# Optimization experiments

Hardware: AMD Instinct MI355X
Metric: run time of the kernel (lower is better)

Reference implementation:

```python
import jax, jax.numpy as jnp
import numpy as np

N = 100000      # num nodes
E = 1600000     # num edges (avg degree 16)
D_IN = 128
D_OUT = 128
EPS = 1e-12     # F.normalize default eps


def setup_inputs() -> dict:
    key = jax.random.key(0)
    k1, k2, k3, k4 = jax.random.split(key, 4)
    x = jax.random.normal(k1, (N, D_IN), dtype=jnp.float32)
    row = jax.random.randint(k2, (E,), 0, N, dtype=jnp.int32)
    # guarantee no self loops in the raw graph: col = (row + offset) % N, offset in [1, N)
    offset = jax.random.randint(k3, (E,), 1, N, dtype=jnp.int32)
    col = (row + offset) % N
    edge_index = jnp.stack([row, col], axis=0)
    # xavier_uniform_ for weight [in, out]
    a = np.sqrt(6.0 / (D_IN + D_OUT)).astype(np.float32)
    weight = jax.random.uniform(k4, (D_IN, D_OUT), dtype=jnp.float32, minval=-a, maxval=a)
    return {"x": x, "edge_index": edge_index, "weight": weight}


def reference(x, edge_index, weight):
    row, col = edge_index[0], edge_index[1]
    # remove_self_loops: drop edges with row == col (mask keeps shapes static)
    mask = (row != col)
    # linear transform first (as in the original forward)
    xw = jnp.matmul(x, weight)                               # [N, D_OUT]
    # scatter_mean over edges with self loops added:
    # out[i] = (sum_{j->i, j!=i} xw[j] + xw[i]) / (deg_nonself(i) + 1)
    msg = jnp.where(mask[:, None], xw[col], jnp.float32(0.0))  # [E, D_OUT]
    seg_sum = jax.ops.segment_sum(msg, row, num_segments=N) + xw
    cnt = jax.ops.segment_sum(mask.astype(xw.dtype), row, num_segments=N) + jnp.float32(1.0)
    out = seg_sum / cnt[:, None]
    # F.normalize(out, p=2, dim=-1): out / max(||out||_2, eps)
    norm = jnp.sqrt(jnp.sum(out * out, axis=-1, keepdims=True))
    out = out / jnp.maximum(norm, jnp.float32(EPS))
    return out
```

## Files before the change

### kernel.cpp

```cpp
#include <hip/hip_runtime.h>
#include <hip/hip_fp16.h>
#include <stdint.h>

#define NN 100000
#define NE 1600000
#define DD 128
#define NTP 100032

#define NBKT 391
#define CAPB 4480
#define GCAP 1024

typedef _Float16 f16x8 __attribute__((ext_vector_type(8)));
typedef float f32x4 __attribute__((ext_vector_type(4)));

__device__ __forceinline__ uint32_t hadd2u(uint32_t a, uint32_t b){
  union { uint32_t u; __half2 h; } x, y;
  x.u = a; y.u = b;
  x.h = __hadd2(x.h, y.h);
  return x.u;
}
__device__ __forceinline__ uint32_t hmul2u(uint32_t a, __half2 m){
  union { uint32_t u; __half2 h; } x; x.u = a;
  x.h = __hmul2(x.h, m);
  return x.u;
}

__global__ __launch_bounds__(256) void k_convert(
    const float4* __restrict__ x, uint2* __restrict__ x16,
    const float* __restrict__ w, uint16_t* __restrict__ wsw){
  int b = blockIdx.x, t = threadIdx.x;
  if (b < 12500){
    int i = b*256 + t;
    float4 v = x[i];
    union { _Float16 h[4]; uint2 u; } r;
    r.h[0] = (_Float16)v.x; r.h[1] = (_Float16)v.y;
    r.h[2] = (_Float16)v.z; r.h[3] = (_Float16)v.w;
    x16[i] = r.u;
  } else {
    int wi = (b - 12500)*256 + t;
    int j = wi & 7, l = (wi >> 3) & 63, kt = (wi >> 9) & 3, ct = wi >> 11;
    int k = kt*32 + ((l >> 4) & 3)*8 + j;
    int d = ct*16 + (l & 15);
    union { _Float16 h; uint16_t u; } cv; cv.h = (_Float16)w[k*DD + d];
    wsw[wi] = cv.u;
  }
}

__global__ __launch_bounds__(256) void k_part1(const int* __restrict__ ei,
                                               int* __restrict__ bktres,
                                               uint32_t* __restrict__ ibuf){
  __shared__ int sh[NBKT];
  int t = threadIdx.x;
  int e0 = blockIdx.x*4096;
  for (int i=t; i<NBKT; i+=256) sh[i] = 0;
  __syncthreads();
  int rr[16], cc[16];
  #pragma unroll
  for (int j=0;j<16;j++){
    int e = e0 + j*256 + t;
    rr[j] = -1;
    if (e < NE){
      rr[j] = ei[e]; cc[j] = ei[NE + e];
      atomicAdd(&sh[rr[j] >> 8], 1);
    }
  }
  __syncthreads();
  for (int i=t; i<NBKT; i+=256){
    int v = sh[i];
    sh[i] = v ? atomicAdd(&bktres[i*16], v) : 0;
  }
  __syncthreads();
  #pragma unroll
  for (int j=0;j<16;j++){
    if (rr[j] >= 0){
      int bk = rr[j] >> 8;
      int p = atomicAdd(&sh[bk], 1);
      if (p < CAPB)
        ibuf[(size_t)bk*CAPB + p] = (uint32_t)(((rr[j] & 255) << 17) | cc[j]);
    }
  }
}

__global__ __launch_bounds__(256) void k_part2(const int* __restrict__ bktres,
                                               uint32_t* __restrict__ ibuf,
                                               uint32_t* __restrict__ rowinfo){
  __shared__ uint32_t s_rec[CAPB];
  __shared__ int s_deg[256], s_off[256], s_cur[256];
  int t = threadIdx.x, lane = t & 63, wid = t >> 6;
  int b = blockIdx.x;
  int cnt = bktres[b*16]; if (cnt > CAPB) cnt = CAPB;
  size_t bb = (size_t)b*CAPB;
  s_deg[t] = 0;
  __syncthreads();
  for (int i=t; i<cnt; i+=256){
    uint32_t rec = ibuf[bb + i];
    s_rec[i] = rec;
    atomicAdd(&s_deg[rec >> 17], 1);
  }
  __syncthreads();
  if (wid == 0){
    int carry = 0;
    for (int ch=0; ch<4; ch++){
      int idx = ch*64 + lane;
      int o = s_deg[idx], v = o;
      #pragma unroll
      for (int d=1; d<64; d<<=1){ int y = __shfl_up(v, d); if (lane >= d) v += y; }
      int ex = carry + v - o;
      s_off[idx] = ex; s_cur[idx] = ex;
      carry += __shfl(v, 63);
    }
  }
  __syncthreads();
  int dgc = s_deg[t] > 255 ? 255 : s_deg[t];
  rowinfo[b*256 + t] = ((uint32_t)s_off[t] << 8) | (uint32_t)dgc;
  for (int i=t; i<cnt; i+=256){
    uint32_t rec = s_rec[i];
    int p = atomicAdd(&s_cur[rec >> 17], 1);
    ibuf[bb + p] = rec & 0x1FFFFu;
  }
}

__global__ __launch_bounds__(256) void k_bin_gather(
    const uint2* __restrict__ xp, const uint32_t* __restrict__ ibuf,
    const uint32_t* __restrict__ rowinfo, uint16_t* __restrict__ agg){
  __shared__ int s_col[GCAP];
  __shared__ int s_loc[32], s_deg[32];
  int t = threadIdx.x, wid = t >> 6, lane = t & 63;
  int b = blockIdx.x;
  int row0 = b << 5;
  if (t < 32){
    uint32_t info = rowinfo[row0 + t];
    s_loc[t] = (int)(info >> 8);
    s_deg[t] = (int)(info & 255u);
  }
  __syncthreads();
  int base = s_loc[0];
  int len = s_loc[31] + s_deg[31] - base; if (len > GCAP) len = GCAP;
  size_t bb = (size_t)(row0 >> 8)*CAPB + base;
  for (int i=t; i<len; i+=256) s_col[i] = (int)ibuf[bb + i];
  __syncthreads();
  int q = lane & 31, half = lane >> 5;
  for (int lr = wid; lr < 32; lr += 4){
    int n = row0 + lr;
    int dg  = s_deg[lr];
    int off = s_loc[lr] - base;
    uint2 sv = xp[(size_t)n*32 + q];
    uint32_t a01 = 0u, a23 = 0u;
    int j = 0;
    for (; j+16 <= dg; j += 16){
      int c0 = s_col[off+j+half],    c1 = s_col[off+j+2+half];
      int c2 = s_col[off+j+4+half],  c3 = s_col[off+j+6+half];
      int c4 = s_col[off+j+8+half],  c5 = s_col[off+j+10+half];
      int c6 = s_col[off+j+12+half], c7 = s_col[off+j+14+half];
      uint2 v0 = xp[(size_t)c0*32 + q]; uint2 v1 = xp[(size_t)c1*32 + q];
      uint2 v2 = xp[(size_t)c2*32 + q]; uint2 v3 = xp[(size_t)c3*32 + q];
      uint2 v4 = xp[(size_t)c4*32 + q]; uint2 v5 = xp[(size_t)c5*32 + q];
      uint2 v6 = xp[(size_t)c6*32 + q]; uint2 v7 = xp[(size_t)c7*32 + q];
      a01 = hadd2u(a01, v0.x); a23 = hadd2u(a23, v0.y);
      a01 = hadd2u(a01, v1.x); a23 = hadd2u(a23, v1.y);
      a01 = hadd2u(a01, v2.x); a23 = hadd2u(a23, v2.y);
      a01 = hadd2u(a01, v3.x); a23 = hadd2u(a23, v3.y);
      a01 = hadd2u(a01, v4.x); a23 = hadd2u(a23, v4.y);
      a01 = hadd2u(a01, v5.x); a23 = hadd2u(a23, v5.y);
      a01 = hadd2u(a01, v6.x); a23 = hadd2u(a23, v6.y);
      a01 = hadd2u(a01, v7.x); a23 = hadd2u(a23, v7.y);
    }
    for (; j+8 <= dg; j += 8){
      int c0 = s_col[off+j+half],   c1 = s_col[off+j+2+half];
      int c2 = s_col[off+j+4+half], c3 = s_col[off+j+6+half];
      uint2 v0 = xp[(size_t)c0*32 + q]; uint2 v1 = xp[(size_t)c1*32 + q];
      uint2 v2 = xp[(size_t)c2*32 + q]; uint2 v3 = xp[(size_t)c3*32 + q];
      a01 = hadd2u(a01, v0.x); a23 = hadd2u(a23, v0.y);
      a01 = hadd2u(a01, v1.x); a23 = hadd2u(a23, v1.y);
      a01 = hadd2u(a01, v2.x); a23 = hadd2u(a23, v2.y);
      a01 = hadd2u(a01, v3.x); a23 = hadd2u(a23, v3.y);
    }
    for (; j+2 <= dg; j += 2){
      int c0 = s_col[off+j+half];
      uint2 v0 = xp[(size_t)c0*32 + q];
      a01 = hadd2u(a01, v0.x); a23 = hadd2u(a23, v0.y);
    }
    if (j < dg){
      int c0 = s_col[off+j];
      uint2 v0 = xp[(size_t)c0*32 + q];
      a01 = hadd2u(a01, half ? 0u : v0.x);
      a23 = hadd2u(a23, half ? 0u : v0.y);
    }
    a01 = hadd2u(a01, (uint32_t)__shfl_xor((int)a01, 32));
    a23 = hadd2u(a23, (uint32_t)__shfl_xor((int)a23, 32));
    __half2 inv2 = __float2half2_rn(1.0f / (float)(dg + 1));
    uint32_t r01 = hmul2u(hadd2u(a01, sv.x), inv2);
    uint32_t r23 = hmul2u(hadd2u(a23, sv.y), inv2);
    uint32_t pair = half ? r23 : r01;
    int k0 = q*4 + half*2;
    int kt = k0 >> 5, gk = (k0 >> 3) & 3, jj = k0 & 7;
    int ld = (n & 15) + (gk << 4);
    *(uint32_t*)(agg + ((((size_t)(n >> 4)*4 + kt)*64 + ld)*8 + jj)) = pair;
  }
}

__global__ __launch_bounds__(256) void k_gemm(const uint16_t* __restrict__ agg,
                                              const uint16_t* __restrict__ wsw,
                                              float* __restrict__ out){
  int tid = threadIdx.x, wid = tid >> 6, lane = tid & 63;
  int g = blockIdx.x*4 + wid;
  const f16x8* A = (const f16x8*)agg;
  const f16x8* B = (const f16x8*)wsw;
  size_t ab = (size_t)g*256 + lane;
  f16x8 a0 = A[ab], a1 = A[ab+64], a2 = A[ab+128], a3 = A[ab+192];

  f32x4 acc[8];
  #pragma unroll
  for (int ct=0;ct<8;ct++) acc[ct] = (f32x4){0.f,0.f,0.f,0.f};
  #pragma unroll
  for (int ct=0;ct<8;ct++){
    acc[ct] = __builtin_amdgcn_mfma_f32_16x16x32_f16(a0, B[(ct*4+0)*64 + lane], acc[ct], 0, 0, 0);
    acc[ct] = __builtin_amdgcn_mfma_f32_16x16x32_f16(a1, B[(ct*4+1)*64 + lane], acc[ct], 0, 0, 0);
    acc[ct] = __builtin_amdgcn_mfma_f32_16x16x32_f16(a2, B[(ct*4+2)*64 + lane], acc[ct], 0, 0, 0);
    acc[ct] = __builtin_amdgcn_mfma_f32_16x16x32_f16(a3, B[(ct*4+3)*64 + lane], acc[ct], 0, 0, 0);
  }

  float sq[4] = {0.f,0.f,0.f,0.f};
  #pragma unroll
  for (int ct=0;ct<8;ct++){
    #pragma unroll
    for (int i=0;i<4;i++) sq[i] += acc[ct][i]*acc[ct][i];
  }
  #pragma unroll
  for (int m=1;m<16;m<<=1){
    #pragma unroll
    for (int i=0;i<4;i++) sq[i] += __shfl_xor(sq[i], m);
  }
  float sc[4];
  #pragma unroll
  for (int i=0;i<4;i++) sc[i] = 1.0f / fmaxf(sqrtf(sq[i]), 1e-12f);

  int col = lane & 15;
  int rb = g*16 + ((lane >> 4) << 2);
  #pragma unroll
  for (int i=0;i<4;i++){
    int n = rb + i;
    if (n < NN){
      #pragma unroll
      for (int ct=0;ct<8;ct++)
        out[(size_t)n*DD + (ct<<4) + col] = acc[ct][i]*sc[i];
    }
  }
}

extern "C" void kernel_launch(void* const* d_in, const int* in_sizes, int n_in,
                              void* d_out, int out_size, void* d_ws, size_t ws_size,
                              hipStream_t stream){
  const float* x = (const float*)d_in[0];
  const int*  ei = (const int*)d_in[1];
  const float* w = (const float*)d_in[2];
  float* out = (float*)d_out;
  char* ws = (char*)d_ws;
  (void)in_sizes; (void)n_in; (void)out_size; (void)ws_size;

  size_t off = 0;
  uint16_t* x16 = (uint16_t*)(ws + off); off += (size_t)NN*DD*2;
  uint16_t* agg = (uint16_t*)(ws + off); off += (size_t)NTP*DD*2;
  uint16_t* wsw = (uint16_t*)(ws + off); off += (size_t)DD*DD*2;
  uint32_t* ibuf = (uint32_t*)(ws + off); off += (size_t)NBKT*CAPB*4;
  int* bktres   = (int*)(ws + off); off += (size_t)NBKT*16*4;
  uint32_t* rowinfo = (uint32_t*)(ws + off); off += (size_t)NBKT*256*4;

  hipMemsetAsync(bktres, 0, (size_t)NBKT*16*4, stream);
  k_convert<<<12564, 256, 0, stream>>>((const float4*)x, (uint2*)x16, w, wsw);
  k_part1<<<391, 256, 0, stream>>>(ei, bktres, ibuf);
  k_part2<<<391, 256, 0, stream>>>(bktres, ibuf, rowinfo);
  k_bin_gather<<<3125, 256, 0, stream>>>((const uint2*)x16, ibuf, rowinfo, agg);
  k_gemm<<<1563, 256, 0, stream>>>(agg, wsw, out);
}
```

Measured before the change: 144.1 us.

## Fuse gather with GEMM through shared memory and merge partition with convert

Merges the fp16 convert kernel with the edge-bucketing pass into one launch. The neighbour-mean gather now also performs the MFMA GEMM and L2 normalisation, keeping the aggregated tile in LDS instead of writing it to global memory and reading it back. Each pair of waves splits the output columns, and partial row norms are combined through shared memory. The gather inner loop is also widened to 32 edges per step, with more loads in flight. This removes two launches and a global round-trip, at the cost of extra LDS, an added barrier, and more register pressure in the gather.

```diff
diff --git a/kernel.cpp b/kernel.cpp
--- a/kernel.cpp
+++ b/kernel.cpp
@@ -5,10 +5,10 @@
 #define NN 100000
 #define NE 1600000
 #define DD 128
-#define NTP 100032
 
 #define NBKT 391
 #define CAPB 4480
+#define NBIN 3125
 #define GCAP 1024
 
 typedef _Float16 f16x8 __attribute__((ext_vector_type(8)));
@@ -26,59 +26,55 @@
   return x.u;
 }
 
-__global__ __launch_bounds__(256) void k_convert(
+__global__ __launch_bounds__(256) void k_front(
+    const int* __restrict__ ei, int* __restrict__ bktres, uint32_t* __restrict__ ibuf,
     const float4* __restrict__ x, uint2* __restrict__ x16,
     const float* __restrict__ w, uint16_t* __restrict__ wsw){
   int b = blockIdx.x, t = threadIdx.x;
-  if (b < 12500){
-    int i = b*256 + t;
+  if (b < NBKT){
+    __shared__ int sh[NBKT];
+    int e0 = b*4096;
+    for (int i=t; i<NBKT; i+=256) sh[i] = 0;
+    __syncthreads();
+    int rr[16], cc[16];
+    #pragma unroll
+    for (int j=0;j<16;j++){
+      int e = e0 + j*256 + t;
+      rr[j] = -1;
+      if (e < NE){
+        rr[j] = ei[e]; cc[j] = ei[NE + e];
+        atomicAdd(&sh[rr[j] >> 8], 1);
+      }
+    }
+    __syncthreads();
+    for (int i=t; i<NBKT; i+=256){
+      int v = sh[i];
+      sh[i] = v ? atomicAdd(&bktres[i*16], v) : 0;
+    }
+    __syncthreads();
+    #pragma unroll
+    for (int j=0;j<16;j++){
+      if (rr[j] >= 0){
+        int bk = rr[j] >> 8;
+        int p = atomicAdd(&sh[bk], 1);
+        if (p < CAPB)
+          ibuf[(size_t)bk*CAPB + p] = (uint32_t)(((rr[j] & 255) << 17) | cc[j]);
+      }
+    }
+  } else if (b < 12891){
+    int i = (b - NBKT)*256 + t;
     float4 v = x[i];
     union { _Float16 h[4]; uint2 u; } r;
     r.h[0] = (_Float16)v.x; r.h[1] = (_Float16)v.y;
     r.h[2] = (_Float16)v.z; r.h[3] = (_Float16)v.w;
     x16[i] = r.u;
   } else {
-    int wi = (b - 12500)*256 + t;
+    int wi = (b - 12891)*256 + t;
     int j = wi & 7, l = (wi >> 3) & 63, kt = (wi >> 9) & 3, ct = wi >> 11;
     int k = kt*32 + ((l >> 4) & 3)*8 + j;
     int d = ct*16 + (l & 15);
     union { _Float16 h; uint16_t u; } cv; cv.h = (_Float16)w[k*DD + d];
     wsw[wi] = cv.u;
-  }
-}
-
-__global__ __launch_bounds__(256) void k_part1(const int* __restrict__ ei,
-                                               int* __restrict__ bktres,
-                                               uint32_t* __restrict__ ibuf){
-  __shared__ int sh[NBKT];
-  int t = threadIdx.x;
-  int e0 = blockIdx.x*4096;
-  for (int i=t; i<NBKT; i+=256) sh[i] = 0;
-  __syncthreads();
-  int rr[16], cc[16];
-  #pragma unroll
-  for (int j=0;j<16;j++){
-    int e = e0 + j*256 + t;
-    rr[j] = -1;
-    if (e < NE){
-      rr[j] = ei[e]; cc[j] = ei[NE + e];
-      atomicAdd(&sh[rr[j] >> 8], 1);
-    }
-  }
-  __syncthreads();
-  for (int i=t; i<NBKT; i+=256){
-    int v = sh[i];
-    sh[i] = v ? atomicAdd(&bktres[i*16], v) : 0;
-  }
-  __syncthreads();
-  #pragma unroll
-  for (int j=0;j<16;j++){
-    if (rr[j] >= 0){
-      int bk = rr[j] >> 8;
-      int p = atomicAdd(&sh[bk], 1);
-      if (p < CAPB)
-        ibuf[(size_t)bk*CAPB + p] = (uint32_t)(((rr[j] & 255) << 17) | cc[j]);
-    }
   }
 }
 
@@ -121,11 +117,14 @@
   }
 }
 
-__global__ __launch_bounds__(256) void k_bin_gather(
+__global__ __launch_bounds__(256) void k_gather_gemm(
     const uint2* __restrict__ xp, const uint32_t* __restrict__ ibuf,
-    const uint32_t* __restrict__ rowinfo, uint16_t* __restrict__ agg){
+    const uint32_t* __restrict__ rowinfo, const uint16_t* __restrict__ wsw,
+    float* __restrict__ out){
   __shared__ int s_col[GCAP];
   __shared__ int s_loc[32], s_deg[32];
+  __shared__ uint16_t sAgg[4096];
+  __shared__ float sSq[2][2][4][4];
   int t = threadIdx.x, wid = t >> 6, lane = t & 63;
   int b = blockIdx.x;
   int row0 = b << 5;
@@ -140,6 +139,7 @@
   size_t bb = (size_t)(row0 >> 8)*CAPB + base;
   for (int i=t; i<len; i+=256) s_col[i] = (int)ibuf[bb + i];
   __syncthreads();
+
   int q = lane & 31, half = lane >> 5;
   for (int lr = wid; lr < 32; lr += 4){
     int n = row0 + lr;
@@ -148,23 +148,15 @@
     uint2 sv = xp[(size_t)n*32 + q];
     uint32_t a01 = 0u, a23 = 0u;
     int j = 0;
-    for (; j+16 <= dg; j += 16){
-      int c0 = s_col[off+j+half],    c1 = s_col[off+j+2+half];
-      int c2 = s_col[off+j+4+half],  c3 = s_col[off+j+6+half];
-      int c4 = s_col[off+j+8+half],  c5 = s_col[off+j+10+half];
-      int c6 = s_col[off+j+12+half], c7 = s_col[off+j+14+half];
-      uint2 v0 = xp[(size_t)c0*32 + q]; uint2 v1 = xp[(size_t)c1*32 + q];
-      uint2 v2 = xp[(size_t)c2*32 + q]; uint2 v3 = xp[(size_t)c3*32 + q];
-      uint2 v4 = xp[(size_t)c4*32 + q]; uint2 v5 = xp[(size_t)c5*32 + q];
-      uint2 v6 = xp[(size_t)c6*32 + q]; uint2 v7 = xp[(size_t)c7*32 + q];
-      a01 = hadd2u(a01, v0.x); a23 = hadd2u(a23, v0.y);
-      a01 = hadd2u(a01, v1.x); a23 = hadd2u(a23, v1.y);
-      a01 = hadd2u(a01, v2.x); a23 = hadd2u(a23, v2.y);
-      a01 = hadd2u(a01, v3.x); a23 = hadd2u(a23, v3.y);
-      a01 = hadd2u(a01, v4.x); a23 = hadd2u(a23, v4.y);
-      a01 = hadd2u(a01, v5.x); a23 = hadd2u(a23, v5.y);
-      a01 = hadd2u(a01, v6.x); a23 = hadd2u(a23, v6.y);
-      a01 = hadd2u(a01, v7.x); a23 = hadd2u(a23, v7.y);
+    for (; j+32 <= dg; j += 32){
+      int cI[16];
+      #pragma unroll
+      for (int u=0; u<16; u++) cI[u] = s_col[off + j + 2*u + half];
+      uint2 vI[16];
+      #pragma unroll
+      for (int u=0; u<16; u++) vI[u] = xp[(size_t)cI[u]*32 + q];
+      #pragma unroll
+      for (int u=0; u<16; u++){ a01 = hadd2u(a01, vI[u].x); a23 = hadd2u(a23, vI[u].y); }
     }
     for (; j+8 <= dg; j += 8){
       int c0 = s_col[off+j+half],   c1 = s_col[off+j+2+half];
@@ -195,57 +187,58 @@
     uint32_t pair = half ? r23 : r01;
     int k0 = q*4 + half*2;
     int kt = k0 >> 5, gk = (k0 >> 3) & 3, jj = k0 & 7;
-    int ld = (n & 15) + (gk << 4);
-    *(uint32_t*)(agg + ((((size_t)(n >> 4)*4 + kt)*64 + ld)*8 + jj)) = pair;
-  }
-}
-
-__global__ __launch_bounds__(256) void k_gemm(const uint16_t* __restrict__ agg,
-                                              const uint16_t* __restrict__ wsw,
-                                              float* __restrict__ out){
-  int tid = threadIdx.x, wid = tid >> 6, lane = tid & 63;
-  int g = blockIdx.x*4 + wid;
-  const f16x8* A = (const f16x8*)agg;
-  const f16x8* B = (const f16x8*)wsw;
-  size_t ab = (size_t)g*256 + lane;
-  f16x8 a0 = A[ab], a1 = A[ab+64], a2 = A[ab+128], a3 = A[ab+192];
-
-  f32x4 acc[8];
-  #pragma unroll
-  for (int ct=0;ct<8;ct++) acc[ct] = (f32x4){0.f,0.f,0.f,0.f};
-  #pragma unroll
-  for (int ct=0;ct<8;ct++){
-    acc[ct] = __builtin_amdgcn_mfma_f32_16x16x32_f16(a0, B[(ct*4+0)*64 + lane], acc[ct], 0, 0, 0);
-    acc[ct] = __builtin_amdgcn_mfma_f32_16x16x32_f16(a1, B[(ct*4+1)*64 + lane], acc[ct], 0, 0, 0);
-    acc[ct] = __builtin_amdgcn_mfma_f32_16x16x32_f16(a2, B[(ct*4+2)*64 + lane], acc[ct], 0, 0, 0);
-    acc[ct] = __builtin_amdgcn_mfma_f32_16x16x32_f16(a3, B[(ct*4+3)*64 + lane], acc[ct], 0, 0, 0);
-  }
-
+    int ld = (lr & 15) + (gk << 4);
+    int lg = lr >> 4;
+    *(uint32_t*)&sAgg[((lg*4 + kt)*64 + ld)*8 + jj] = pair;
+  }
+  __syncthreads();
+
+  int g2 = wid >> 1, ch = (wid & 1)*4;
+  const f16x8* Bf = (const f16x8*)wsw;
+  f16x8 a0 = *(const f16x8*)&sAgg[((g2*4+0)*64 + lane)*8];
+  f16x8 a1 = *(const f16x8*)&sAgg[((g2*4+1)*64 + lane)*8];
+  f16x8 a2 = *(const f16x8*)&sAgg[((g2*4+2)*64 + lane)*8];
+  f16x8 a3 = *(const f16x8*)&sAgg[((g2*4+3)*64 + lane)*8];
+  f32x4 acc[4];
+  #pragma unroll
+  for (int c2=0;c2<4;c2++) acc[c2] = (f32x4){0.f,0.f,0.f,0.f};
+  #pragma unroll
+  for (int c2=0;c2<4;c2++){
+    acc[c2] = __builtin_amdgcn_mfma_f32_16x16x32_f16(a0, Bf[((ch+c2)*4+0)*64 + lane], acc[c2], 0, 0, 0);
+    acc[c2] = __builtin_amdgcn_mfma_f32_16x16x32_f16(a1, Bf[((ch+c2)*4+1)*64 + lane], acc[c2], 0, 0, 0);
+    acc[c2] = __builtin_amdgcn_mfma_f32_16x16x32_f16(a2, Bf[((ch+c2)*4+2)*64 + lane], acc[c2], 0, 0, 0);
+    acc[c2] = __builtin_amdgcn_mfma_f32_16x16x32_f16(a3, Bf[((ch+c2)*4+3)*64 + lane], acc[c2], 0, 0, 0);
+  }
   float sq[4] = {0.f,0.f,0.f,0.f};
   #pragma unroll
-  for (int ct=0;ct<8;ct++){
-    #pragma unroll
-    for (int i=0;i<4;i++) sq[i] += acc[ct][i]*acc[ct][i];
+  for (int c2=0;c2<4;c2++){
+    #pragma unroll
+    for (int i=0;i<4;i++) sq[i] += acc[c2][i]*acc[c2][i];
   }
   #pragma unroll
   for (int m=1;m<16;m<<=1){
     #pragma unroll
     for (int i=0;i<4;i++) sq[i] += __shfl_xor(sq[i], m);
   }
+  if ((lane & 15) == 0){
+    #pragma unroll
+    for (int i=0;i<4;i++) sSq[g2][wid & 1][lane >> 4][i] = sq[i];
+  }
+  __syncthreads();
   float sc[4];
   #pragma unroll
-  for (int i=0;i<4;i++) sc[i] = 1.0f / fmaxf(sqrtf(sq[i]), 1e-12f);
-
+  for (int i=0;i<4;i++){
+    float tot = sq[i] + sSq[g2][(wid & 1) ^ 1][lane >> 4][i];
+    sc[i] = 1.0f / fmaxf(sqrtf(tot), 1e-12f);
+  }
   int col = lane & 15;
-  int rb = g*16 + ((lane >> 4) << 2);
+  int rb = row0 + g2*16 + ((lane >> 4) << 2);
   #pragma unroll
   for (int i=0;i<4;i++){
     int n = rb + i;
-    if (n < NN){
-      #pragma unroll
-      for (int ct=0;ct<8;ct++)
-        out[(size_t)n*DD + (ct<<4) + col] = acc[ct][i]*sc[i];
-    }
+    #pragma unroll
+    for (int c2=0;c2<4;c2++)
+      out[(size_t)n*DD + (ch + c2)*16 + col] = acc[c2][i]*sc[i];
   }
 }
 
@@ -261,16 +254,13 @@
 
   size_t off = 0;
   uint16_t* x16 = (uint16_t*)(ws + off); off += (size_t)NN*DD*2;
-  uint16_t* agg = (uint16_t*)(ws + off); off += (size_t)NTP*DD*2;
   uint16_t* wsw = (uint16_t*)(ws + off); off += (size_t)DD*DD*2;
   uint32_t* ibuf = (uint32_t*)(ws + off); off += (size_t)NBKT*CAPB*4;
   int* bktres   = (int*)(ws + off); off += (size_t)NBKT*16*4;
   uint32_t* rowinfo = (uint32_t*)(ws + off); off += (size_t)NBKT*256*4;
 
   hipMemsetAsync(bktres, 0, (size_t)NBKT*16*4, stream);
-  k_convert<<<12564, 256, 0, stream>>>((const float4*)x, (uint2*)x16, w, wsw);
-  k_part1<<<391, 256, 0, stream>>>(ei, bktres, ibuf);
-  k_part2<<<391, 256, 0, stream>>>(bktres, ibuf, rowinfo);
-  k_bin_gather<<<3125, 256, 0, stream>>>((const uint2*)x16, ibuf, rowinfo, agg);
-  k_gemm<<<1563, 256, 0, stream>>>(agg, wsw, out);
-}
+  k_front<<<12955, 256, 0, stream>>>(ei, bktres, ibuf, (const float4*)x, (uint2*)x16, w, wsw);
+  k_part2<<<NBKT, 256, 0, stream>>>(bktres, ibuf, rowinfo);
+  k_gather_gemm<<<NBIN, 256, 0, stream>>>((const uint2*)x16, ibuf, rowinfo, wsw, out);
+}
```

Result: faster. 139.0 us (-3.5%).

## Fuse edge partition into convert kernel and use row-major agg layout

Applied to the files above, without the earlier changes.

Merges the edge bucketing pass (part1) into the fp16 conversion kernel as extra blocks, so one launch does partitioning, x conversion and weight swizzle, which removes a launch and lets the two independent jobs overlap. The gather now writes aggregated rows in plain row-major order instead of the MFMA-swizzled tile layout, and the GEMM loads its A fragments straight from row-major memory. The padded agg buffer goes away, and the GEMM drops its row bounds check in favour of an early exit for waves past the last tile. The row-major A loads are strided per lane, which may coalesce less well than the old contiguous swizzled fragments.

```diff
diff --git a/kernel.cpp b/kernel.cpp
--- a/kernel.cpp
+++ b/kernel.cpp
@@ -5,10 +5,10 @@
 #define NN 100000
 #define NE 1600000
 #define DD 128
-#define NTP 100032
 
 #define NBKT 391
 #define CAPB 4480
+#define NBIN 3125
 #define GCAP 1024
 
 typedef _Float16 f16x8 __attribute__((ext_vector_type(8)));
@@ -26,59 +26,55 @@
   return x.u;
 }
 
-__global__ __launch_bounds__(256) void k_convert(
+__global__ __launch_bounds__(256) void k_front(
+    const int* __restrict__ ei, int* __restrict__ bktres, uint32_t* __restrict__ ibuf,
     const float4* __restrict__ x, uint2* __restrict__ x16,
     const float* __restrict__ w, uint16_t* __restrict__ wsw){
   int b = blockIdx.x, t = threadIdx.x;
-  if (b < 12500){
-    int i = b*256 + t;
+  if (b < NBKT){
+    __shared__ int sh[NBKT];
+    int e0 = b*4096;
+    for (int i=t; i<NBKT; i+=256) sh[i] = 0;
+    __syncthreads();
+    int rr[16], cc[16];
+    #pragma unroll
+    for (int j=0;j<16;j++){
+      int e = e0 + j*256 + t;
+      rr[j] = -1;
+      if (e < NE){
+        rr[j] = ei[e]; cc[j] = ei[NE + e];
+        atomicAdd(&sh[rr[j] >> 8], 1);
+      }
+    }
+    __syncthreads();
+    for (int i=t; i<NBKT; i+=256){
+      int v = sh[i];
+      sh[i] = v ? atomicAdd(&bktres[i*16], v) : 0;
+    }
+    __syncthreads();
+    #pragma unroll
+    for (int j=0;j<16;j++){
+      if (rr[j] >= 0){
+        int bk = rr[j] >> 8;
+        int p = atomicAdd(&sh[bk], 1);
+        if (p < CAPB)
+          ibuf[(size_t)bk*CAPB + p] = (uint32_t)(((rr[j] & 255) << 17) | cc[j]);
+      }
+    }
+  } else if (b < 12891){
+    int i = (b - NBKT)*256 + t;
     float4 v = x[i];
     union { _Float16 h[4]; uint2 u; } r;
     r.h[0] = (_Float16)v.x; r.h[1] = (_Float16)v.y;
     r.h[2] = (_Float16)v.z; r.h[3] = (_Float16)v.w;
     x16[i] = r.u;
   } else {
-    int wi = (b - 12500)*256 + t;
+    int wi = (b - 12891)*256 + t;
     int j = wi & 7, l = (wi >> 3) & 63, kt = (wi >> 9) & 3, ct = wi >> 11;
     int k = kt*32 + ((l >> 4) & 3)*8 + j;
     int d = ct*16 + (l & 15);
     union { _Float16 h; uint16_t u; } cv; cv.h = (_Float16)w[k*DD + d];
     wsw[wi] = cv.u;
-  }
-}
-
-__global__ __launch_bounds__(256) void k_part1(const int* __restrict__ ei,
-                                               int* __restrict__ bktres,
-                                               uint32_t* __restrict__ ibuf){
-  __shared__ int sh[NBKT];
-  int t = threadIdx.x;
-  int e0 = blockIdx.x*4096;
-  for (int i=t; i<NBKT; i+=256) sh[i] = 0;
-  __syncthreads();
-  int rr[16], cc[16];
-  #pragma unroll
-  for (int j=0;j<16;j++){
-    int e = e0 + j*256 + t;
-    rr[j] = -1;
-    if (e < NE){
-      rr[j] = ei[e]; cc[j] = ei[NE + e];
-      atomicAdd(&sh[rr[j] >> 8], 1);
-    }
-  }
-  __syncthreads();
-  for (int i=t; i<NBKT; i+=256){
-    int v = sh[i];
-    sh[i] = v ? atomicAdd(&bktres[i*16], v) : 0;
-  }
-  __syncthreads();
-  #pragma unroll
-  for (int j=0;j<16;j++){
-    if (rr[j] >= 0){
-      int bk = rr[j] >> 8;
-      int p = atomicAdd(&sh[bk], 1);
-      if (p < CAPB)
-        ibuf[(size_t)bk*CAPB + p] = (uint32_t)(((rr[j] & 255) << 17) | cc[j]);
-    }
   }
 }
 
@@ -121,9 +117,9 @@
   }
 }
 
-__global__ __launch_bounds__(256) void k_bin_gather(
+__global__ __launch_bounds__(256) void k_gather(
     const uint2* __restrict__ xp, const uint32_t* __restrict__ ibuf,
-    const uint32_t* __restrict__ rowinfo, uint16_t* __restrict__ agg){
+    const uint32_t* __restrict__ rowinfo, uint32_t* __restrict__ agg32){
   __shared__ int s_col[GCAP];
   __shared__ int s_loc[32], s_deg[32];
   int t = threadIdx.x, wid = t >> 6, lane = t & 63;
@@ -140,6 +136,7 @@
   size_t bb = (size_t)(row0 >> 8)*CAPB + base;
   for (int i=t; i<len; i+=256) s_col[i] = (int)ibuf[bb + i];
   __syncthreads();
+
   int q = lane & 31, half = lane >> 5;
   for (int lr = wid; lr < 32; lr += 4){
     int n = row0 + lr;
@@ -192,11 +189,7 @@
     __half2 inv2 = __float2half2_rn(1.0f / (float)(dg + 1));
     uint32_t r01 = hmul2u(hadd2u(a01, sv.x), inv2);
     uint32_t r23 = hmul2u(hadd2u(a23, sv.y), inv2);
-    uint32_t pair = half ? r23 : r01;
-    int k0 = q*4 + half*2;
-    int kt = k0 >> 5, gk = (k0 >> 3) & 3, jj = k0 & 7;
-    int ld = (n & 15) + (gk << 4);
-    *(uint32_t*)(agg + ((((size_t)(n >> 4)*4 + kt)*64 + ld)*8 + jj)) = pair;
+    agg32[(size_t)n*64 + (q << 1) + half] = half ? r23 : r01;
   }
 }
 
@@ -205,22 +198,24 @@
                                               float* __restrict__ out){
   int tid = threadIdx.x, wid = tid >> 6, lane = tid & 63;
   int g = blockIdx.x*4 + wid;
-  const f16x8* A = (const f16x8*)agg;
-  const f16x8* B = (const f16x8*)wsw;
-  size_t ab = (size_t)g*256 + lane;
-  f16x8 a0 = A[ab], a1 = A[ab+64], a2 = A[ab+128], a3 = A[ab+192];
+  if (g >= 6250) return;
+  const char* aggb = (const char*)agg;
+  const f16x8* Bf = (const f16x8*)wsw;
+  int row = g*16 + (lane & 15), gk = lane >> 4;
+  f16x8 a[4];
+  #pragma unroll
+  for (int kt=0; kt<4; kt++)
+    a[kt] = *(const f16x8*)(aggb + (size_t)row*256 + kt*64 + gk*16);
 
   f32x4 acc[8];
   #pragma unroll
   for (int ct=0;ct<8;ct++) acc[ct] = (f32x4){0.f,0.f,0.f,0.f};
   #pragma unroll
   for (int ct=0;ct<8;ct++){
-    acc[ct] = __builtin_amdgcn_mfma_f32_16x16x32_f16(a0, B[(ct*4+0)*64 + lane], acc[ct], 0, 0, 0);
-    acc[ct] = __builtin_amdgcn_mfma_f32_16x16x32_f16(a1, B[(ct*4+1)*64 + lane], acc[ct], 0, 0, 0);
-    acc[ct] = __builtin_amdgcn_mfma_f32_16x16x32_f16(a2, B[(ct*4+2)*64 + lane], acc[ct], 0, 0, 0);
-    acc[ct] = __builtin_amdgcn_mfma_f32_16x16x32_f16(a3, B[(ct*4+3)*64 + lane], acc[ct], 0, 0, 0);
-  }
-
+    #pragma unroll
+    for (int kt=0;kt<4;kt++)
+      acc[ct] = __builtin_amdgcn_mfma_f32_16x16x32_f16(a[kt], Bf[(ct*4+kt)*64 + lane], acc[ct], 0, 0, 0);
+  }
   float sq[4] = {0.f,0.f,0.f,0.f};
   #pragma unroll
   for (int ct=0;ct<8;ct++){
@@ -232,20 +227,18 @@
     #pragma unroll
     for (int i=0;i<4;i++) sq[i] += __shfl_xor(sq[i], m);
   }
-  float sc[4];
-  #pragma unroll
-  for (int i=0;i<4;i++) sc[i] = 1.0f / fmaxf(sqrtf(sq[i]), 1e-12f);
+  float sc4[4];
+  #pragma unroll
+  for (int i=0;i<4;i++) sc4[i] = 1.0f / fmaxf(sqrtf(sq[i]), 1e-12f);
 
   int col = lane & 15;
-  int rb = g*16 + ((lane >> 4) << 2);
+  int rb = g*16 + (gk << 2);
   #pragma unroll
   for (int i=0;i<4;i++){
     int n = rb + i;
-    if (n < NN){
-      #pragma unroll
-      for (int ct=0;ct<8;ct++)
-        out[(size_t)n*DD + (ct<<4) + col] = acc[ct][i]*sc[i];
-    }
+    #pragma unroll
+    for (int ct=0;ct<8;ct++)
+      out[(size_t)n*DD + (ct<<4) + col] = acc[ct][i]*sc4[i];
   }
 }
 
@@ -261,16 +254,15 @@
 
   size_t off = 0;
   uint16_t* x16 = (uint16_t*)(ws + off); off += (size_t)NN*DD*2;
-  uint16_t* agg = (uint16_t*)(ws + off); off += (size_t)NTP*DD*2;
+  uint16_t* agg = (uint16_t*)(ws + off); off += (size_t)NN*DD*2;
   uint16_t* wsw = (uint16_t*)(ws + off); off += (size_t)DD*DD*2;
   uint32_t* ibuf = (uint32_t*)(ws + off); off += (size_t)NBKT*CAPB*4;
   int* bktres   = (int*)(ws + off); off += (size_t)NBKT*16*4;
   uint32_t* rowinfo = (uint32_t*)(ws + off); off += (size_t)NBKT*256*4;
 
   hipMemsetAsync(bktres, 0, (size_t)NBKT*16*4, stream);
-  k_convert<<<12564, 256, 0, stream>>>((const float4*)x, (uint2*)x16, w, wsw);
-  k_part1<<<391, 256, 0, stream>>>(ei, bktres, ibuf);
-  k_part2<<<391, 256, 0, stream>>>(bktres, ibuf, rowinfo);
-  k_bin_gather<<<3125, 256, 0, stream>>>((const uint2*)x16, ibuf, rowinfo, agg);
+  k_front<<<12955, 256, 0, stream>>>(ei, bktres, ibuf, (const float4*)x, (uint2*)x16, w, wsw);
+  k_part2<<<NBKT, 256, 0, stream>>>(bktres, ibuf, rowinfo);
+  k_gather<<<NBIN, 256, 0, stream>>>((const uint2*)x16, ibuf, rowinfo, (uint32_t*)agg);
   k_gemm<<<1563, 256, 0, stream>>>(agg, wsw, out);
 }
```

Result: faster. 134.3 us (-6.8%).
